# Kernel optimization log

Measured on AMD Instinct MI355X. Metric: run time of the kernel, lower is better.

Reference implementation:

```python
import jax, jax.numpy as jnp
import numpy as np

D = 1024      # input_dim
H = 4096      # expert_hidden_dim
C = 512       # num_classes
E = 8         # num_experts
K = 2         # top_k
B = 16384     # batch
LN_EPS = 1e-5


def setup_inputs() -> dict:
    key = jax.random.key(0)
    ks = jax.random.split(key, 6)
    scale = 0.02
    return {
        "x": jax.random.normal(ks[0], (B, D), dtype=jnp.float32),
        "gate_w": jax.random.normal(ks[1], (D, E), dtype=jnp.float32) * scale,
        "gate_b": jnp.zeros((E,), dtype=jnp.float32),
        "w1": jax.random.normal(ks[2], (E, D, H), dtype=jnp.float32) * scale,
        "b1": jnp.zeros((E, H), dtype=jnp.float32),
        "ln_g": jnp.ones((E, H), dtype=jnp.float32),
        "ln_b": jnp.zeros((E, H), dtype=jnp.float32),
        "w2": jax.random.normal(ks[3], (E, H, C), dtype=jnp.float32) * scale,
        "b2": jnp.zeros((E, C), dtype=jnp.float32),
    }


def reference(x, gate_w, gate_b, w1, b1, ln_g, ln_b, w2, b2):
    # Router: logits [B,E], top-k over experts, softmax over the k selected logits
    logits = x @ gate_w + gate_b
    top_vals, top_idx = jax.lax.top_k(logits, K)        # [B,K]
    probs = jax.nn.softmax(top_vals, axis=1)            # [B,K]

    # Combined gate weight per (token, expert): replaces the nested k/expert
    # mask-gather-scatter loops; top_idx rows have distinct experts, so this
    # is exactly sum_k probs[:,k] * (top_idx[:,k]==e). [B,E]
    n = x.shape[0]
    weight = jnp.zeros((n, E), dtype=x.dtype).at[jnp.arange(n)[:, None], top_idx].add(probs)

    out = jnp.zeros((n, C), dtype=x.dtype)
    for e in range(E):  # fixed small expert count; each expert has distinct params
        h = x @ w1[e] + b1[e]                           # [B,H]
        mu = jnp.mean(h, axis=-1, keepdims=True)
        var = jnp.var(h, axis=-1, keepdims=True)
        h = (h - mu) * jax.lax.rsqrt(var + LN_EPS) * ln_g[e] + ln_b[e]
        h = jax.nn.gelu(h, approximate=False)           # torch GELU default = erf
        # Dropout is identity in eval mode.
        out = out + weight[:, e:e + 1] * (h @ w2[e] + b2[e])
    return out, logits
```

## Files before the change

kernel.cpp:

```cpp
#include <hip/hip_runtime.h>
#include <hip/hip_bf16.h>
#include <cstdint>

#define DEV __device__ __forceinline__

constexpr int Bt = 16384;
constexpr int Dd = 1024;
constexpr int Hh = 4096;
constexpr int Cc = 512;
constexpr int Ee = 8;
constexpr int PCAP = 34816;

typedef short bf16x8 __attribute__((ext_vector_type(8)));
typedef ushort u16x8 __attribute__((ext_vector_type(8)));
typedef float f32x4  __attribute__((ext_vector_type(4)));

DEV ushort f2bf(float f){
  uint32_t u = __float_as_uint(f);
  u += 0x7fffu + ((u >> 16) & 1u);
  return (ushort)(u >> 16);
}
DEV float bf2f(ushort u){ return __uint_as_float(((uint32_t)u) << 16); }

DEV float gelu_t(float x){
  float x2 = x * x;
  float z = x * (0.7978845608f + 0.0356774081f * x2);
  float t = __builtin_amdgcn_exp2f(z * -2.8853900818f);
  return x * __builtin_amdgcn_rcpf(1.f + t);
}

typedef const __attribute__((address_space(1))) void* gptr_t;
typedef __attribute__((address_space(3))) void* lptr_t;
DEV void gload_lds16(const void* g, void* l){
  __builtin_amdgcn_global_load_lds((gptr_t)g, (lptr_t)l, 16, 0, 0);
}

#define BARRIER() __builtin_amdgcn_s_barrier()
#define LGKM0()  do { asm volatile("s_waitcnt lgkmcnt(0)" ::: "memory"); \
                      __builtin_amdgcn_sched_barrier(0); } while(0)
#define WAITV(N) asm volatile("s_waitcnt vmcnt(" #N ")" ::: "memory")

__global__ __launch_bounds__(256) void k_router(
    const float* __restrict__ x, const float* __restrict__ gw,
    const float* __restrict__ gb, float* __restrict__ logits,
    int2* __restrict__ topi, float2* __restrict__ topp)
{
  __shared__ float lgwT[Ee * Dd];
  int tid = threadIdx.x;
  const float4* gw4 = (const float4*)gw;
  for (int i = tid; i < Dd * Ee / 4; i += 256){
    float4 v = gw4[i];
    int d = i >> 1, e0 = (i & 1) * 4;
    lgwT[(e0 + 0) * Dd + d] = v.x;
    lgwT[(e0 + 1) * Dd + d] = v.y;
    lgwT[(e0 + 2) * Dd + d] = v.z;
    lgwT[(e0 + 3) * Dd + d] = v.w;
  }
  __syncthreads();
  int wv = tid >> 6, lane = tid & 63;
  int t = blockIdx.x * 4 + wv;
  const float* xr = x + (size_t)t * Dd;
  float acc[Ee];
  #pragma unroll
  for (int e = 0; e < Ee; e++) acc[e] = 0.f;
  for (int i = 0; i < Dd / 64; i++){
    int d = i * 64 + lane;
    float xs = xr[d];
    #pragma unroll
    for (int e = 0; e < Ee; e++) acc[e] += xs * lgwT[e * Dd + d];
  }
  #pragma unroll
  for (int e = 0; e < Ee; e++){
    #pragma unroll
    for (int m = 1; m < 64; m <<= 1) acc[e] += __shfl_xor(acc[e], m, 64);
  }
  if (lane == 0){
    float lg[Ee];
    #pragma unroll
    for (int e = 0; e < Ee; e++) lg[e] = acc[e] + gb[e];
    #pragma unroll
    for (int e = 0; e < Ee; e++) logits[(size_t)t * Ee + e] = lg[e];
    int i0 = 0; float v0 = lg[0];
    #pragma unroll
    for (int e = 1; e < Ee; e++) if (lg[e] > v0){ v0 = lg[e]; i0 = e; }
    int i1 = (i0 == 0) ? 1 : 0; float v1 = lg[i1];
    #pragma unroll
    for (int e = 0; e < Ee; e++) if (e != i0 && lg[e] > v1){ v1 = lg[e]; i1 = e; }
    float ex = expf(v1 - v0);
    float p0 = 1.f / (1.f + ex);
    float p1 = ex * p0;
    topi[t] = make_int2(i0, i1);
    topp[t] = make_float2(p0, p1);
  }
}

__global__ __launch_bounds__(256) void k_offsets(
    const int2* __restrict__ topi, int* __restrict__ off)
{
  __shared__ int part[4][8];
  int tid = threadIdx.x, lane = tid & 63, w = tid >> 6;
  int c0 = 0, c1 = 0, c2 = 0, c3 = 0, c4 = 0, c5 = 0, c6 = 0, c7 = 0;
  for (int t = tid; t < Bt; t += 256){
    int2 ii = topi[t];
    c0 += (ii.x == 0) + (ii.y == 0);
    c1 += (ii.x == 1) + (ii.y == 1);
    c2 += (ii.x == 2) + (ii.y == 2);
    c3 += (ii.x == 3) + (ii.y == 3);
    c4 += (ii.x == 4) + (ii.y == 4);
    c5 += (ii.x == 5) + (ii.y == 5);
    c6 += (ii.x == 6) + (ii.y == 6);
    c7 += (ii.x == 7) + (ii.y == 7);
  }
  #pragma unroll
  for (int m = 1; m < 64; m <<= 1){
    c0 += __shfl_xor(c0, m, 64); c1 += __shfl_xor(c1, m, 64);
    c2 += __shfl_xor(c2, m, 64); c3 += __shfl_xor(c3, m, 64);
    c4 += __shfl_xor(c4, m, 64); c5 += __shfl_xor(c5, m, 64);
    c6 += __shfl_xor(c6, m, 64); c7 += __shfl_xor(c7, m, 64);
  }
  if (lane == 0){
    part[w][0] = c0; part[w][1] = c1; part[w][2] = c2; part[w][3] = c3;
    part[w][4] = c4; part[w][5] = c5; part[w][6] = c6; part[w][7] = c7;
  }
  __syncthreads();
  if (tid == 0){
    int a = 0;
    for (int e = 0; e < Ee; e++){
      int h = part[0][e] + part[1][e] + part[2][e] + part[3][e];
      off[e] = a; a += ((h + 255) >> 8) << 8;
    }
    off[Ee] = a;
  }
}

__global__ __launch_bounds__(256) void k_scatter(
    const int2* __restrict__ topi, const int* __restrict__ off,
    int* __restrict__ fill, int* __restrict__ ptok, int2* __restrict__ pidx)
{
  __shared__ int lcnt[8], lbase[8];
  int tid = threadIdx.x;
  if (tid < 8) lcnt[tid] = 0;
  __syncthreads();
  int t = blockIdx.x * 256 + tid;
  int2 ii = topi[t];
  int r0 = atomicAdd(&lcnt[ii.x], 1);
  int r1 = atomicAdd(&lcnt[ii.y], 1);
  __syncthreads();
  if (tid < 8) lbase[tid] = off[tid] + atomicAdd(&fill[tid], lcnt[tid]);
  __syncthreads();
  int p0 = lbase[ii.x] + r0;
  int p1 = lbase[ii.y] + r1;
  ptok[p0] = t;
  ptok[p1] = t;
  pidx[t] = make_int2(p0, p1);
}

__global__ __launch_bounds__(256) void k_cvt_bf16(
    const float* __restrict__ in, ushort* __restrict__ outp, int n4)
{
  int i = blockIdx.x * 256 + threadIdx.x;
  if (i >= n4) return;
  float4 v = ((const float4*)in)[i];
  ushort4 o; o.x = f2bf(v.x); o.y = f2bf(v.y); o.z = f2bf(v.z); o.w = f2bf(v.w);
  ((ushort4*)outp)[i] = o;
}

__global__ __launch_bounds__(256) void k_transpose_bf16(
    const float* __restrict__ in, ushort* __restrict__ outp, int R, int Cd)
{
  __shared__ float tl[64][65];
  size_t eoff = (size_t)blockIdx.z * (size_t)R * (size_t)Cd;
  int c0 = blockIdx.x * 64, r0 = blockIdx.y * 64;
  int tid = threadIdx.x;
  int r = tid >> 2, cq = tid & 3;
  const float* src = in + eoff + (size_t)(r0 + r) * Cd + c0 + cq * 16;
  #pragma unroll
  for (int q = 0; q < 4; q++){
    float4 v = ((const float4*)src)[q];
    int cc = cq * 16 + q * 4;
    tl[r][cc + 0] = v.x; tl[r][cc + 1] = v.y; tl[r][cc + 2] = v.z; tl[r][cc + 3] = v.w;
  }
  __syncthreads();
  int c = tid >> 2, rq = tid & 3;
  ushort* dst = outp + eoff + (size_t)(c0 + c) * R + r0 + rq * 16;
  #pragma unroll
  for (int q = 0; q < 4; q++){
    ushort4 o;
    o.x = f2bf(tl[rq * 16 + q * 4 + 0][c]);
    o.y = f2bf(tl[rq * 16 + q * 4 + 1][c]);
    o.z = f2bf(tl[rq * 16 + q * 4 + 2][c]);
    o.w = f2bf(tl[rq * 16 + q * 4 + 3][c]);
    ((ushort4*)dst)[q] = o;
  }
}


template<int QM>
DEV void read_a(bf16x8 (&aq)[4][2], const char* lb, int wm, const uint32_t (&alane)[2]){
  #pragma unroll
  for (int i = 0; i < 4; i++)
    #pragma unroll
    for (int ks = 0; ks < 2; ks++)
      aq[i][ks] = *(const bf16x8*)(lb + wm * 16384 + QM * 8192 + i * 2048 + alane[ks]);
}
template<int QN>
DEV void read_b(bf16x8 (&bq)[4][2], const char* lb, int wn, const uint32_t (&alane)[2]){
  #pragma unroll
  for (int j = 0; j < 2; j++)
    #pragma unroll
    for (int ks = 0; ks < 2; ks++)
      bq[QN * 2 + j][ks] = *(const bf16x8*)(lb + 32768 + (wn >> 1) * 16384 +
                              (wn & 1) * 8192 + QN * 4096 + j * 2048 + alane[ks]);
}
template<int QM, int QN>
DEV void mfma_quad(f32x4 (&acc)[8][4], const bf16x8 (&aq)[4][2], const bf16x8 (&bq)[4][2]){
  #pragma unroll
  for (int i = 0; i < 4; i++)
    #pragma unroll
    for (int j = 0; j < 2; j++)
      #pragma unroll
      for (int ks = 0; ks < 2; ks++)
        acc[QM * 4 + i][QN * 2 + j] = __builtin_amdgcn_mfma_f32_16x16x32_bf16(
            aq[i][ks], bq[QN * 2 + j][ks], acc[QM * 4 + i][QN * 2 + j], 0, 0, 0);
}
DEV void stage4(const char* gb, const uint32_t (&src)[2][2], uint32_t ko, char* dst){
  gload_lds16(gb + src[0][0] + ko, dst);
  gload_lds16(gb + src[0][1] + ko, dst + 8192);
  gload_lds16(gb + src[1][0] + ko, dst + 16384);
  gload_lds16(gb + src[1][1] + ko, dst + 16384 + 8192);
}

template<int MODE, int Kd, int Nd>
__global__ __launch_bounds__(512, 2) void k_gemm8(
    const ushort* __restrict__ A, const ushort* __restrict__ Bm,
    const float* __restrict__ bias, const int* __restrict__ off,
    const int* __restrict__ ptok, ushort* __restrict__ Outp, int chunk_base)
{
  __shared__ char lds[131072];
  constexpr int NTk = Kd / 64;
  constexpr int NTn = Nd / 256;
  int nwg = gridDim.x;
  int orig = blockIdx.x;
  int q = nwg >> 3, r8 = nwg & 7;
  int xcd = orig & 7, lin = orig >> 3;
  int swz = (xcd < r8 ? xcd * (q + 1) : r8 * (q + 1) + (xcd - r8) * q) + lin;
  int mcount = nwg / NTn;
  int r0l = (swz % mcount) * 256;
  int n0 = (swz / mcount) * 256;
  int grow0 = chunk_base + r0l;
  if (grow0 >= off[8]) return;

  int tid = threadIdx.x;
  int e = 0;
  #pragma unroll
  for (int i = 1; i < 8; i++) e = (grow0 >= off[i]) ? i : e;

  uint32_t sx = (uint32_t)(((tid & 7) ^ ((tid >> 3) & 7)) << 4);
  int rh0 = tid >> 3, rh1 = rh0 + 64;
  uint32_t a_src[2][2], b_src[2][2];
  #pragma unroll
  for (int h = 0; h < 2; h++){
    int ra0 = h * 128 + rh0, ra1 = h * 128 + rh1;
    uint32_t rowb0, rowb1;
    if (MODE == 0){
      rowb0 = (uint32_t)ptok[grow0 + ra0] * (uint32_t)(Kd * 2);
      rowb1 = (uint32_t)ptok[grow0 + ra1] * (uint32_t)(Kd * 2);
    } else {
      rowb0 = (uint32_t)(r0l + ra0) * (uint32_t)(Kd * 2);
      rowb1 = (uint32_t)(r0l + ra1) * (uint32_t)(Kd * 2);
    }
    a_src[h][0] = rowb0 + sx;
    a_src[h][1] = rowb1 + sx;
    b_src[h][0] = (uint32_t)(e * Nd + n0 + ra0) * (uint32_t)(Kd * 2) + sx;
    b_src[h][1] = (uint32_t)(e * Nd + n0 + ra1) * (uint32_t)(Kd * 2) + sx;
  }
  const char* Ab = (const char*)A;
  const char* Bb = (const char*)Bm;
  int w = tid >> 6, lane = tid & 63;
  int wm = w >> 2, wn = w & 3;
  int l15 = lane & 15, lhi = lane >> 4;
  char* wdst = lds + w * 1024;

  uint32_t alane[2];
  #pragma unroll
  for (int ks = 0; ks < 2; ks++)
    alane[ks] = (uint32_t)(l15 * 128 + (((ks * 4 + lhi) ^ (l15 & 7)) << 4));

  f32x4 acc[8][4];
  #pragma unroll
  for (int mi = 0; mi < 8; mi++)
    #pragma unroll
    for (int ni = 0; ni < 4; ni++) acc[mi][ni] = (f32x4){0.f, 0.f, 0.f, 0.f};
  bf16x8 aq[4][2], bq[4][2];

  stage4(Ab, a_src, 0u, wdst);
  stage4(Bb, b_src, 0u, wdst + 32768);
  stage4(Ab, a_src, 128u, wdst + 65536);
  stage4(Bb, b_src, 128u, wdst + 65536 + 32768);
  WAITV(8);
  BARRIER();

  #pragma unroll 1
  for (int t = 0; t < NTk; ++t){
    char* lb = lds + (t & 1) * 65536;
    char* wlb = wdst + (t & 1) * 65536;
    uint32_t ko2 = (uint32_t)(t + 2) * 128u;
    read_a<0>(aq, lb, wm, alane);
    read_b<0>(bq, lb, wn, alane);
    BARRIER(); LGKM0();
    __builtin_amdgcn_s_setprio(1);
    mfma_quad<0, 0>(acc, aq, bq);
    __builtin_amdgcn_s_setprio(0);
    BARRIER();
    read_b<1>(bq, lb, wn, alane);
    BARRIER(); LGKM0();
    __builtin_amdgcn_s_setprio(1);
    mfma_quad<0, 1>(acc, aq, bq);
    __builtin_amdgcn_s_setprio(0);
    BARRIER();
    read_a<1>(aq, lb, wm, alane);
    if (t + 2 < NTk) stage4(Bb, b_src, ko2, wlb + 32768);
    BARRIER(); LGKM0();
    __builtin_amdgcn_s_setprio(1);
    mfma_quad<1, 1>(acc, aq, bq);
    __builtin_amdgcn_s_setprio(0);
    BARRIER();
    if (t + 2 < NTk) stage4(Ab, a_src, ko2, wlb);
    BARRIER();
    __builtin_amdgcn_s_setprio(1);
    mfma_quad<1, 0>(acc, aq, bq);
    __builtin_amdgcn_s_setprio(0);
    if (t + 2 < NTk)      { WAITV(8); }
    else if (t + 1 < NTk) { WAITV(0); }
    BARRIER();
  }

  float bv[4]; int nn[4];
  #pragma unroll
  for (int ni = 0; ni < 4; ni++){
    nn[ni] = n0 + wn * 64 + ni * 16 + l15;
    bv[ni] = bias[e * Nd + nn[ni]];
  }
  #pragma unroll
  for (int mi = 0; mi < 8; mi++){
    #pragma unroll
    for (int r = 0; r < 4; r++){
      int rl = r0l + wm * 128 + mi * 16 + lhi * 4 + r;
      size_t rowbase = (MODE == 0) ? (size_t)rl * Nd
                                   : (size_t)(chunk_base + rl) * Nd;
      #pragma unroll
      for (int ni = 0; ni < 4; ni++){
        float v = acc[mi][ni][r] + bv[ni];
        Outp[rowbase + nn[ni]] = f2bf(v);
      }
    }
  }
}

__global__ __launch_bounds__(256) void k_lngelu(
    ushort* __restrict__ h, const int* __restrict__ off,
    const float* __restrict__ lng, const float* __restrict__ lnb, int chunk_base)
{
  __shared__ float redS[8];
  int rl = blockIdx.x, tid = threadIdx.x;
  int grow = chunk_base + rl;
  if (grow >= off[8]) return;
  int e = 0;
  #pragma unroll
  for (int i = 1; i < 8; i++) e = (grow >= off[i]) ? i : e;
  ushort* hr = h + (size_t)rl * Hh;
  float xv[16];
  #pragma unroll
  for (int i = 0; i < 4; i++){
    int c = i * 256 + tid;
    ushort4 v = *(const ushort4*)(hr + c * 4);
    xv[i * 4 + 0] = bf2f(v.x); xv[i * 4 + 1] = bf2f(v.y);
    xv[i * 4 + 2] = bf2f(v.z); xv[i * 4 + 3] = bf2f(v.w);
  }
  float s0 = 0.f, s1 = 0.f;
  #pragma unroll
  for (int i = 0; i < 16; i++){ s0 += xv[i]; s1 += xv[i] * xv[i]; }
  #pragma unroll
  for (int m = 1; m < 64; m <<= 1){ s0 += __shfl_xor(s0, m, 64); s1 += __shfl_xor(s1, m, 64); }
  int w = tid >> 6;
  if ((tid & 63) == 0){ redS[w * 2] = s0; redS[w * 2 + 1] = s1; }
  __syncthreads();
  s0 = redS[0] + redS[2] + redS[4] + redS[6];
  s1 = redS[1] + redS[3] + redS[5] + redS[7];
  float mu = s0 * (1.f / 4096.f);
  float var = s1 * (1.f / 4096.f) - mu * mu;
  float rs = rsqrtf(var + 1e-5f);
  const float4* gp = (const float4*)(lng + (size_t)e * Hh);
  const float4* bp = (const float4*)(lnb + (size_t)e * Hh);
  #pragma unroll
  for (int i = 0; i < 4; i++){
    int c = i * 256 + tid;
    float4 g = gp[c], b = bp[c];
    float v0 = (xv[i * 4 + 0] - mu) * rs * g.x + b.x;
    float v1 = (xv[i * 4 + 1] - mu) * rs * g.y + b.y;
    float v2 = (xv[i * 4 + 2] - mu) * rs * g.z + b.z;
    float v3 = (xv[i * 4 + 3] - mu) * rs * g.w + b.w;
    ushort4 o;
    o.x = f2bf(gelu_t(v0)); o.y = f2bf(gelu_t(v1));
    o.z = f2bf(gelu_t(v2)); o.w = f2bf(gelu_t(v3));
    *(ushort4*)(hr + c * 4) = o;
  }
}

__global__ __launch_bounds__(128) void k_combine(
    const ushort* __restrict__ y, const int2* __restrict__ pidx,
    const float2* __restrict__ topp, float* __restrict__ outp)
{
  int t = blockIdx.x;
  int c4 = threadIdx.x << 2;
  int2 pi = pidx[t]; float2 pp = topp[t];
  ushort4 a = *(const ushort4*)(y + (size_t)pi.x * Cc + c4);
  ushort4 b = *(const ushort4*)(y + (size_t)pi.y * Cc + c4);
  float4 o;
  o.x = pp.x * bf2f(a.x) + pp.y * bf2f(b.x);
  o.y = pp.x * bf2f(a.y) + pp.y * bf2f(b.y);
  o.z = pp.x * bf2f(a.z) + pp.y * bf2f(b.z);
  o.w = pp.x * bf2f(a.w) + pp.y * bf2f(b.w);
  *(float4*)(outp + (size_t)t * Cc + c4) = o;
}

extern "C" void kernel_launch(void* const* d_in, const int* in_sizes, int n_in,
                              void* d_out, int out_size, void* d_ws, size_t ws_size,
                              hipStream_t stream)
{
  const float* x   = (const float*)d_in[0];
  const float* gw  = (const float*)d_in[1];
  const float* gb  = (const float*)d_in[2];
  const float* w1  = (const float*)d_in[3];
  const float* b1  = (const float*)d_in[4];
  const float* lng = (const float*)d_in[5];
  const float* lnb = (const float*)d_in[6];
  const float* w2  = (const float*)d_in[7];
  const float* b2  = (const float*)d_in[8];
  float* outp   = (float*)d_out;
  float* logits = outp + (size_t)Bt * Cc;

  char* p = (char*)d_ws;
  auto alloc = [&](size_t bytes) -> char* {
    char* q = p; p += (bytes + 255) & ~(size_t)255; return q;
  };
  int*    ctrl  = (int*)alloc(256);
  int* fill = ctrl + 8; int* off = ctrl + 16;
  int2*   topi  = (int2*)alloc((size_t)Bt * 8);
  float2* topp  = (float2*)alloc((size_t)Bt * 8);
  int2*   pidx  = (int2*)alloc((size_t)Bt * 8);
  int*    ptok  = (int*)alloc((size_t)PCAP * 4);
  ushort* ybuf  = (ushort*)alloc((size_t)PCAP * Cc * 2);
  ushort* xb    = (ushort*)alloc((size_t)Bt * Dd * 2);
  ushort* w1t   = (ushort*)alloc((size_t)Ee * Hh * Dd * 2);
  ushort* w2t   = (ushort*)alloc((size_t)Ee * Cc * Hh * 2);
  size_t used  = (size_t)(p - (char*)d_ws);
  size_t avail = ws_size > used ? ws_size - used : 0;
  long long chr = (long long)(avail / ((size_t)Hh * 2));
  chr &= ~255LL;
  int CH = (int)(chr < 256 ? 256 : (chr > PCAP ? (long long)PCAP : chr));
  ushort* hbuf = (ushort*)p;

  hipMemsetAsync(ctrl, 0, 256, stream);
  hipMemsetAsync(ptok, 0, (size_t)PCAP * 4, stream);

  k_router<<<Bt / 4, 256, 0, stream>>>(x, gw, gb, logits, topi, topp);
  k_offsets<<<1, 256, 0, stream>>>(topi, off);
  k_scatter<<<Bt / 256, 256, 0, stream>>>(topi, off, fill, ptok, pidx);
  k_cvt_bf16<<<(Bt * Dd / 4) / 256, 256, 0, stream>>>(x, xb, Bt * Dd / 4);
  k_transpose_bf16<<<dim3(Hh / 64, Dd / 64, Ee), 256, 0, stream>>>(w1, w1t, Dd, Hh);
  k_transpose_bf16<<<dim3(Cc / 64, Hh / 64, Ee), 256, 0, stream>>>(w2, w2t, Hh, Cc);

  for (int base = 0; base < PCAP; base += CH){
    int rows = (PCAP - base < CH) ? (PCAP - base) : CH;
    int nb1 = (rows / 256) * (Hh / 256);
    k_gemm8<0, Dd, Hh><<<nb1, 512, 0, stream>>>(xb, w1t, b1, off, ptok, hbuf, base);
    k_lngelu<<<rows, 256, 0, stream>>>(hbuf, off, lng, lnb, base);
    int nb2 = (rows / 256) * (Cc / 256);
    k_gemm8<1, Hh, Cc><<<nb2, 512, 0, stream>>>(hbuf, w2t, b2, off, ptok, ybuf, base);
  }
  k_combine<<<Bt, 128, 0, stream>>>(ybuf, pidx, topp, outp);
}
```

Before: 841.7 us.

## Split-K the second expert GEMM and restructure LDS read pipeline

The down-projection GEMM is split into two K halves, each written to its own bf16 output plane, and the combine kernel sums both planes. This doubles the number of workgroups for the small-N GEMM so more CUs are busy. The GEMM main loop is also reorganized: LDS fragment reads for the next tile are prefetched before the loop and after the barrier, with partial lgkmcnt waits and fewer barriers. The cost is extra y-buffer traffic, an additional bf16 rounding of the partial sums, and the combine kernel reading twice as much data.

```diff
diff --git a/kernel.cpp b/kernel.cpp
--- a/kernel.cpp
+++ b/kernel.cpp
@@ -36,7 +36,7 @@
 }
 
 #define BARRIER() __builtin_amdgcn_s_barrier()
-#define LGKM0()  do { asm volatile("s_waitcnt lgkmcnt(0)" ::: "memory"); \
+#define WAITL(N) do { asm volatile("s_waitcnt lgkmcnt(" #N ")" ::: "memory"); \
                       __builtin_amdgcn_sched_barrier(0); } while(0)
 #define WAITV(N) asm volatile("s_waitcnt vmcnt(" #N ")" ::: "memory")
 
@@ -195,33 +195,32 @@
 }
 
 
-template<int QM>
-DEV void read_a(bf16x8 (&aq)[4][2], const char* lb, int wm, const uint32_t (&alane)[2]){
+DEV void read_Aq(bf16x8 (&aq)[4][2], const char* lb, int abase, const uint32_t (&alane)[2]){
   #pragma unroll
   for (int i = 0; i < 4; i++)
     #pragma unroll
-    for (int ks = 0; ks < 2; ks++)
-      aq[i][ks] = *(const bf16x8*)(lb + wm * 16384 + QM * 8192 + i * 2048 + alane[ks]);
-}
-template<int QN>
-DEV void read_b(bf16x8 (&bq)[4][2], const char* lb, int wn, const uint32_t (&alane)[2]){
+    for (int k2 = 0; k2 < 2; k2++)
+      aq[i][k2] = *(const bf16x8*)(lb + abase + i * 2048 + alane[k2]);
+}
+template<int P>
+DEV void read_Bp(bf16x8 (&bq)[4][2], const char* lb, int wn, const uint32_t (&alane)[2]){
   #pragma unroll
   for (int j = 0; j < 2; j++)
     #pragma unroll
-    for (int ks = 0; ks < 2; ks++)
-      bq[QN * 2 + j][ks] = *(const bf16x8*)(lb + 32768 + (wn >> 1) * 16384 +
-                              (wn & 1) * 8192 + QN * 4096 + j * 2048 + alane[ks]);
-}
-template<int QM, int QN>
-DEV void mfma_quad(f32x4 (&acc)[8][4], const bf16x8 (&aq)[4][2], const bf16x8 (&bq)[4][2]){
+    for (int k2 = 0; k2 < 2; k2++)
+      bq[P * 2 + j][k2] = *(const bf16x8*)(lb + 32768 + (wn >> 1) * 16384 +
+                              (wn & 1) * 8192 + P * 4096 + j * 2048 + alane[k2]);
+}
+template<int MQ, int NB>
+DEV void mfma_half(f32x4 (&acc)[8][4], const bf16x8 (&a)[4][2], const bf16x8 (&b)[4][2]){
   #pragma unroll
   for (int i = 0; i < 4; i++)
     #pragma unroll
     for (int j = 0; j < 2; j++)
       #pragma unroll
-      for (int ks = 0; ks < 2; ks++)
-        acc[QM * 4 + i][QN * 2 + j] = __builtin_amdgcn_mfma_f32_16x16x32_bf16(
-            aq[i][ks], bq[QN * 2 + j][ks], acc[QM * 4 + i][QN * 2 + j], 0, 0, 0);
+      for (int k2 = 0; k2 < 2; k2++)
+        acc[MQ * 4 + i][NB * 2 + j] = __builtin_amdgcn_mfma_f32_16x16x32_bf16(
+            a[i][k2], b[NB * 2 + j][k2], acc[MQ * 4 + i][NB * 2 + j], 0, 0, 0);
 }
 DEV void stage4(const char* gb, const uint32_t (&src)[2][2], uint32_t ko, char* dst){
   gload_lds16(gb + src[0][0] + ko, dst);
@@ -230,23 +229,29 @@
   gload_lds16(gb + src[1][1] + ko, dst + 16384 + 8192);
 }
 
-template<int MODE, int Kd, int Nd>
+template<int MODE, int Kd, int Nd, int KS>
 __global__ __launch_bounds__(512, 2) void k_gemm8(
     const ushort* __restrict__ A, const ushort* __restrict__ Bm,
     const float* __restrict__ bias, const int* __restrict__ off,
-    const int* __restrict__ ptok, ushort* __restrict__ Outp, int chunk_base)
+    const int* __restrict__ ptok, ushort* __restrict__ Outp, int chunk_base,
+    int plane_elems)
 {
   __shared__ char lds[131072];
-  constexpr int NTk = Kd / 64;
+  constexpr int Kh  = Kd / KS;
+  constexpr int NTk = Kh / 64;
   constexpr int NTn = Nd / 256;
   int nwg = gridDim.x;
   int orig = blockIdx.x;
   int q = nwg >> 3, r8 = nwg & 7;
   int xcd = orig & 7, lin = orig >> 3;
   int swz = (xcd < r8 ? xcd * (q + 1) : r8 * (q + 1) + (xcd - r8) * q) + lin;
-  int mcount = nwg / NTn;
-  int r0l = (swz % mcount) * 256;
-  int n0 = (swz / mcount) * 256;
+  int mcount = nwg / (NTn * KS);
+  int m = swz % mcount;
+  int rest = swz / mcount;
+  int nI = rest % NTn, ksI = rest / NTn;
+  int r0l = m * 256;
+  int n0 = nI * 256;
+  uint32_t kbyte = (uint32_t)ksI * (uint32_t)(Kh * 2);
   int grow0 = chunk_base + r0l;
   if (grow0 >= off[8]) return;
 
@@ -269,10 +274,10 @@
       rowb0 = (uint32_t)(r0l + ra0) * (uint32_t)(Kd * 2);
       rowb1 = (uint32_t)(r0l + ra1) * (uint32_t)(Kd * 2);
     }
-    a_src[h][0] = rowb0 + sx;
-    a_src[h][1] = rowb1 + sx;
-    b_src[h][0] = (uint32_t)(e * Nd + n0 + ra0) * (uint32_t)(Kd * 2) + sx;
-    b_src[h][1] = (uint32_t)(e * Nd + n0 + ra1) * (uint32_t)(Kd * 2) + sx;
+    a_src[h][0] = rowb0 + kbyte + sx;
+    a_src[h][1] = rowb1 + kbyte + sx;
+    b_src[h][0] = (uint32_t)(e * Nd + n0 + ra0) * (uint32_t)(Kd * 2) + kbyte + sx;
+    b_src[h][1] = (uint32_t)(e * Nd + n0 + ra1) * (uint32_t)(Kd * 2) + kbyte + sx;
   }
   const char* Ab = (const char*)A;
   const char* Bb = (const char*)Bm;
@@ -280,11 +285,13 @@
   int wm = w >> 2, wn = w & 3;
   int l15 = lane & 15, lhi = lane >> 4;
   char* wdst = lds + w * 1024;
+  int abase0 = wm * 16384;
+  int abase1 = wm * 16384 + 8192;
 
   uint32_t alane[2];
   #pragma unroll
-  for (int ks = 0; ks < 2; ks++)
-    alane[ks] = (uint32_t)(l15 * 128 + (((ks * 4 + lhi) ^ (l15 & 7)) << 4));
+  for (int k2 = 0; k2 < 2; k2++)
+    alane[k2] = (uint32_t)(l15 * 128 + (((k2 * 4 + lhi) ^ (l15 & 7)) << 4));
 
   f32x4 acc[8][4];
   #pragma unroll
@@ -299,48 +306,52 @@
   stage4(Bb, b_src, 128u, wdst + 65536 + 32768);
   WAITV(8);
   BARRIER();
+  read_Aq(aq, lds, abase0, alane);
+  read_Bp<0>(bq, lds, wn, alane);
+  read_Bp<1>(bq, lds, wn, alane);
 
   #pragma unroll 1
   for (int t = 0; t < NTk; ++t){
-    char* lb = lds + (t & 1) * 65536;
+    const char* lb = lds + (t & 1) * 65536;
     char* wlb = wdst + (t & 1) * 65536;
-    uint32_t ko2 = (uint32_t)(t + 2) * 128u;
-    read_a<0>(aq, lb, wm, alane);
-    read_b<0>(bq, lb, wn, alane);
-    BARRIER(); LGKM0();
+    WAITL(4);
     __builtin_amdgcn_s_setprio(1);
-    mfma_quad<0, 0>(acc, aq, bq);
+    mfma_half<0, 0>(acc, aq, bq);
     __builtin_amdgcn_s_setprio(0);
+    WAITL(0);
+    __builtin_amdgcn_s_setprio(1);
+    mfma_half<0, 1>(acc, aq, bq);
+    __builtin_amdgcn_s_setprio(0);
+    read_Aq(aq, lb, abase1, alane);
+    WAITL(0);
     BARRIER();
-    read_b<1>(bq, lb, wn, alane);
-    BARRIER(); LGKM0();
+    if (t + 2 < NTk){
+      uint32_t ko2 = (uint32_t)(t + 2) * 128u;
+      stage4(Ab, a_src, ko2, wlb);
+      stage4(Bb, b_src, ko2, wlb + 32768);
+    }
     __builtin_amdgcn_s_setprio(1);
-    mfma_quad<0, 1>(acc, aq, bq);
-    __builtin_amdgcn_s_setprio(0);
-    BARRIER();
-    read_a<1>(aq, lb, wm, alane);
-    if (t + 2 < NTk) stage4(Bb, b_src, ko2, wlb + 32768);
-    BARRIER(); LGKM0();
-    __builtin_amdgcn_s_setprio(1);
-    mfma_quad<1, 1>(acc, aq, bq);
-    __builtin_amdgcn_s_setprio(0);
-    BARRIER();
-    if (t + 2 < NTk) stage4(Ab, a_src, ko2, wlb);
-    BARRIER();
-    __builtin_amdgcn_s_setprio(1);
-    mfma_quad<1, 0>(acc, aq, bq);
+    mfma_half<1, 1>(acc, aq, bq);
+    mfma_half<1, 0>(acc, aq, bq);
     __builtin_amdgcn_s_setprio(0);
     if (t + 2 < NTk)      { WAITV(8); }
     else if (t + 1 < NTk) { WAITV(0); }
     BARRIER();
+    if (t + 1 < NTk){
+      const char* nb = lds + ((t + 1) & 1) * 65536;
+      read_Aq(aq, nb, abase0, alane);
+      read_Bp<0>(bq, nb, wn, alane);
+      read_Bp<1>(bq, nb, wn, alane);
+    }
   }
 
   float bv[4]; int nn[4];
   #pragma unroll
   for (int ni = 0; ni < 4; ni++){
     nn[ni] = n0 + wn * 64 + ni * 16 + l15;
-    bv[ni] = bias[e * Nd + nn[ni]];
-  }
+    bv[ni] = (MODE == 0 || ksI == 0) ? bias[e * Nd + nn[ni]] : 0.f;
+  }
+  ushort* OutP = Outp + (size_t)ksI * (size_t)plane_elems;
   #pragma unroll
   for (int mi = 0; mi < 8; mi++){
     #pragma unroll
@@ -351,7 +362,7 @@
       #pragma unroll
       for (int ni = 0; ni < 4; ni++){
         float v = acc[mi][ni][r] + bv[ni];
-        Outp[rowbase + nn[ni]] = f2bf(v);
+        OutP[rowbase + nn[ni]] = f2bf(v);
       }
     }
   }
@@ -408,19 +419,21 @@
 }
 
 __global__ __launch_bounds__(128) void k_combine(
-    const ushort* __restrict__ y, const int2* __restrict__ pidx,
+    const ushort* __restrict__ y, int plane, const int2* __restrict__ pidx,
     const float2* __restrict__ topp, float* __restrict__ outp)
 {
   int t = blockIdx.x;
   int c4 = threadIdx.x << 2;
   int2 pi = pidx[t]; float2 pp = topp[t];
-  ushort4 a = *(const ushort4*)(y + (size_t)pi.x * Cc + c4);
-  ushort4 b = *(const ushort4*)(y + (size_t)pi.y * Cc + c4);
+  ushort4 a0 = *(const ushort4*)(y + (size_t)pi.x * Cc + c4);
+  ushort4 a1 = *(const ushort4*)(y + (size_t)plane + (size_t)pi.x * Cc + c4);
+  ushort4 b0 = *(const ushort4*)(y + (size_t)pi.y * Cc + c4);
+  ushort4 b1 = *(const ushort4*)(y + (size_t)plane + (size_t)pi.y * Cc + c4);
   float4 o;
-  o.x = pp.x * bf2f(a.x) + pp.y * bf2f(b.x);
-  o.y = pp.x * bf2f(a.y) + pp.y * bf2f(b.y);
-  o.z = pp.x * bf2f(a.z) + pp.y * bf2f(b.z);
-  o.w = pp.x * bf2f(a.w) + pp.y * bf2f(b.w);
+  o.x = pp.x * (bf2f(a0.x) + bf2f(a1.x)) + pp.y * (bf2f(b0.x) + bf2f(b1.x));
+  o.y = pp.x * (bf2f(a0.y) + bf2f(a1.y)) + pp.y * (bf2f(b0.y) + bf2f(b1.y));
+  o.z = pp.x * (bf2f(a0.z) + bf2f(a1.z)) + pp.y * (bf2f(b0.z) + bf2f(b1.z));
+  o.w = pp.x * (bf2f(a0.w) + bf2f(a1.w)) + pp.y * (bf2f(b0.w) + bf2f(b1.w));
   *(float4*)(outp + (size_t)t * Cc + c4) = o;
 }
 
@@ -440,6 +453,8 @@
   float* outp   = (float*)d_out;
   float* logits = outp + (size_t)Bt * Cc;
 
+  constexpr int YPLANE = PCAP * Cc;
+
   char* p = (char*)d_ws;
   auto alloc = [&](size_t bytes) -> char* {
     char* q = p; p += (bytes + 255) & ~(size_t)255; return q;
@@ -450,7 +465,7 @@
   float2* topp  = (float2*)alloc((size_t)Bt * 8);
   int2*   pidx  = (int2*)alloc((size_t)Bt * 8);
   int*    ptok  = (int*)alloc((size_t)PCAP * 4);
-  ushort* ybuf  = (ushort*)alloc((size_t)PCAP * Cc * 2);
+  ushort* ybuf  = (ushort*)alloc((size_t)YPLANE * 2 * 2);
   ushort* xb    = (ushort*)alloc((size_t)Bt * Dd * 2);
   ushort* w1t   = (ushort*)alloc((size_t)Ee * Hh * Dd * 2);
   ushort* w2t   = (ushort*)alloc((size_t)Ee * Cc * Hh * 2);
@@ -474,10 +489,10 @@
   for (int base = 0; base < PCAP; base += CH){
     int rows = (PCAP - base < CH) ? (PCAP - base) : CH;
     int nb1 = (rows / 256) * (Hh / 256);
-    k_gemm8<0, Dd, Hh><<<nb1, 512, 0, stream>>>(xb, w1t, b1, off, ptok, hbuf, base);
+    k_gemm8<0, Dd, Hh, 1><<<nb1, 512, 0, stream>>>(xb, w1t, b1, off, ptok, hbuf, base, 0);
     k_lngelu<<<rows, 256, 0, stream>>>(hbuf, off, lng, lnb, base);
-    int nb2 = (rows / 256) * (Cc / 256);
-    k_gemm8<1, Hh, Cc><<<nb2, 512, 0, stream>>>(hbuf, w2t, b2, off, ptok, ybuf, base);
-  }
-  k_combine<<<Bt, 128, 0, stream>>>(ybuf, pidx, topp, outp);
-}
+    int nb2 = (rows / 256) * (Cc / 256) * 2;
+    k_gemm8<1, Hh, Cc, 2><<<nb2, 512, 0, stream>>>(hbuf, w2t, b2, off, ptok, ybuf, base, YPLANE);
+  }
+  k_combine<<<Bt, 128, 0, stream>>>(ybuf, YPLANE, pidx, topp, outp);
+}
```

New measurement: 771.8 us. 1.09x faster.
